# Optimization experiments

Hardware: AMD Instinct MI355X
Metric: run time of the kernel (lower is better)

The kernel has to match this reference:

```python
import jax, jax.numpy as jnp
import numpy as np

L, E, TOP_K = 3, 8, 2
B, N, D, DS = 256, 1024, 512, 128

def setup_inputs() -> dict:
    key = jax.random.key(0)
    ks = jax.random.split(key, 10)
    s = 0.05  # weight init scale
    return {
        "token": jax.random.normal(ks[0], (B, 1, D), jnp.float32),
        "node_emb": jax.random.normal(ks[1], (B, N, D), jnp.float32),
        "states": jnp.zeros((L, E, B, DS), jnp.float32),
        "Wg": jax.random.normal(ks[2], (L, D, E), jnp.float32) * s,
        "bg": jnp.zeros((L, E), jnp.float32),
        "A": jax.random.normal(ks[3], (L, E, DS), jnp.float32),
        "Bin": jax.random.normal(ks[4], (L, E, D, DS), jnp.float32) * s,
        "Cout": jax.random.normal(ks[5], (L, E, DS, D), jnp.float32) * s,
        "Dsk": jax.random.normal(ks[6], (L, E, D), jnp.float32) * s,
        "Wq": jax.random.normal(ks[7], (D, D), jnp.float32) * s,
        "bq": jnp.zeros((D,), jnp.float32),
    }

def reference(token, node_emb, states, Wg, bg, A, Bin, Cout, Dsk, Wq, bq):
    # token: (B,1,D) -> h: (B,D)
    h = token[:, 0, :]
    lb_loss = jnp.float32(0.0)
    new_states = []
    for l in range(L):
        # --- MoE router: top-k softmax gating ---
        probs = jax.nn.softmax(h @ Wg[l] + bg[l])              # (B,E)
        topv, topi = jax.lax.top_k(probs, TOP_K)               # (B,k)
        gates_k = topv / jnp.sum(topv, axis=-1, keepdims=True)  # renormalized
        oh = jax.nn.one_hot(topi, E, dtype=probs.dtype)        # (B,k,E)
        gate_full = jnp.einsum('bk,bke->be', gates_k, oh)      # (B,E)
        sel = jnp.sum(oh, axis=1) > 0                          # (B,E) bool
        # --- state-space experts (computed densely for all experts) ---
        s = states[l]                                          # (E,B,DS)
        decay = jax.nn.sigmoid(A[l])[:, None, :]               # (E,1,DS)
        s_new = decay * s + jnp.einsum('bd,eds->ebs', h, Bin[l])   # (E,B,DS)
        y = jnp.einsum('ebs,esd->ebd', s_new, Cout[l]) + h[None] * Dsk[l][:, None, :]
        out = jnp.einsum('be,ebd->bd', gate_full, y)           # weighted combine
        # only routed experts advance their state
        keep = sel.T[:, :, None]                               # (E,B,1)
        new_states.append(jnp.where(keep, s_new, s))
        # load-balance loss: E * sum_e mean(probs_e) * mean(frac routed to e)
        lb_loss = lb_loss + E * jnp.sum(jnp.mean(probs, axis=0) * jnp.mean(sel.astype(probs.dtype), axis=0))
        h = h + out                                            # residual
    # --- query projection + logits over nodes ---
    q = h @ Wq + bq                                            # (B,D)
    logits = jnp.einsum('bd,bnd->bn', q, node_emb) / jnp.sqrt(jnp.float32(D))
    return logits, jnp.stack(new_states), lb_loss
```

## Files before the change

kernel.cpp:

```cpp
#include <hip/hip_runtime.h>
#include <math.h>

#define LNUM 3
#define ENUM 8
#define TOPK 2
#define BSZ 256
#define NSZ 1024
#define DSZ 512
#define SSZ 128

typedef float f32x4 __attribute__((ext_vector_type(4)));

__global__ __launch_bounds__(1024, 2) void mega_kernel(
    const float* __restrict__ token,
    const float* __restrict__ node_emb,
    const float* __restrict__ states,
    const float* __restrict__ Wg,
    const float* __restrict__ bg,
    const float* __restrict__ A,
    const float* __restrict__ Bin,
    const float* __restrict__ Cout,
    const float* __restrict__ Dsk,
    const float* __restrict__ Wq,
    const float* __restrict__ bq,
    float* __restrict__ out_logits,
    float* __restrict__ out_states,
    float* __restrict__ acc)
{
    const int b = blockIdx.x;
    const int t = threadIdx.x;
    const int wave = t >> 6;
    const int lane = t & 63;

    __shared__ float h_s[DSZ];
    __shared__ float yacc_s[DSZ];
    __shared__ float snew_s[TOPK][SSZ];
    __shared__ float logit_s[ENUM];
    __shared__ f32x4 part4[1024];
    float* part = (float*)part4;

    if (t < DSZ) h_s[t] = token[b * DSZ + t];

    for (int l = 0; l < LNUM; ++l) {
        const float* Wg_l  = Wg  + (size_t)l * DSZ * ENUM;
        const float* bg_l  = bg  + (size_t)l * ENUM;
        const float* A_l   = A   + (size_t)l * ENUM * SSZ;
        const float* Bin_l = Bin + (size_t)l * ENUM * DSZ * SSZ;
        const float* Cou_l = Cout+ (size_t)l * ENUM * SSZ * DSZ;
        const float* Dsk_l = Dsk + (size_t)l * ENUM * DSZ;
        const float* st_l  = states     + (size_t)l * ENUM * BSZ * SSZ;
        float*       os_l  = out_states + (size_t)l * ENUM * BSZ * SSZ;

        __syncthreads();
        part4[t] = ((const f32x4*)Wg_l)[t];
        __syncthreads();

        if (wave < ENUM) {
            float p = 0.f;
            #pragma unroll
            for (int i = 0; i < 8; ++i) {
                const int d = lane + i * 64;
                p = fmaf(h_s[d], part[d * ENUM + wave], p);
            }
            for (int off = 32; off; off >>= 1) p += __shfl_down(p, off, 64);
            if (lane == 0) logit_s[wave] = p + bg_l[wave];
        }
        __syncthreads();

        float probs[ENUM];
        float mx = logit_s[0];
        for (int e = 1; e < ENUM; ++e) mx = fmaxf(mx, logit_s[e]);
        float ssum = 0.f;
        for (int e = 0; e < ENUM; ++e) { probs[e] = expf(logit_s[e] - mx); ssum += probs[e]; }
        const float sinv = 1.f / ssum;
        for (int e = 0; e < ENUM; ++e) probs[e] *= sinv;

        int i0 = 0;
        for (int e = 1; e < ENUM; ++e) if (probs[e] > probs[i0]) i0 = e;
        int i1 = -1;
        for (int e = 0; e < ENUM; ++e) {
            if (e == i0) continue;
            if (i1 < 0 || probs[e] > probs[i1]) i1 = e;
        }
        float g0 = probs[i0], g1 = probs[i1];
        const float ginv = 1.f / (g0 + g1);
        g0 *= ginv; g1 *= ginv;

        if (t < ENUM) {
            atomicAdd(&acc[(l * 2 + 0) * ENUM + t], probs[t]);
            atomicAdd(&acc[(l * 2 + 1) * ENUM + t], (t == i0 || t == i1) ? 1.0f : 0.0f);
        }

        #pragma unroll
        for (int k = 0; k < TOPK; ++k) {
            const int e = k ? i1 : i0;
            {
                const int c  = t >> 5;
                const int sq = t & 31;
                const float* Bp = Bin_l + (size_t)e * DSZ * SSZ + sq * 4;
                const int d0 = c * 16;
                f32x4 acc4 = {0.f, 0.f, 0.f, 0.f};
                #pragma unroll
                for (int d = 0; d < 16; ++d)
                    acc4 += *(const f32x4*)(Bp + (size_t)(d0 + d) * SSZ) * h_s[d0 + d];
                part4[c * 32 + sq] = acc4;
            }
            __syncthreads();
            if (t < SSZ) {
                float sum = 0.f;
                #pragma unroll
                for (int c = 0; c < 32; ++c) sum += part[c * 128 + t];
                const float a = A_l[e * SSZ + t];
                const float decay = 1.f / (1.f + expf(-a));
                snew_s[k][t] = decay * st_l[((size_t)e * BSZ + b) * SSZ + t] + sum;
            }
            __syncthreads();
        }

        {
            const int e = t >> 7, s = t & 127;
            float v;
            if (e == i0)      v = snew_s[0][s];
            else if (e == i1) v = snew_s[1][s];
            else              v = st_l[((size_t)e * BSZ + b) * SSZ + s];
            os_l[((size_t)e * BSZ + b) * SSZ + s] = v;
        }

        #pragma unroll
        for (int k = 0; k < TOPK; ++k) {
            const int e = k ? i1 : i0;
            const float g = k ? g1 : g0;
            {
                const int sc = t >> 7;
                const int dq = t & 127;
                const float* Cp = Cou_l + (size_t)e * SSZ * DSZ + dq * 4;
                const float* sp = snew_s[k];
                const int s0 = sc * 16;
                f32x4 acc4 = {0.f, 0.f, 0.f, 0.f};
                #pragma unroll
                for (int s = 0; s < 16; ++s)
                    acc4 += *(const f32x4*)(Cp + (size_t)(s0 + s) * DSZ) * sp[s0 + s];
                part4[sc * 128 + dq] = acc4;
            }
            __syncthreads();
            if (t < DSZ) {
                float yk = 0.f;
                #pragma unroll
                for (int sc = 0; sc < 8; ++sc) yk += part[sc * 512 + t];
                const float hd = h_s[t];
                yk = g * (yk + hd * Dsk_l[e * DSZ + t]);
                if (k == 0) yacc_s[t] = yk;
                else        h_s[t] = hd + yacc_s[t] + yk;
            }
            __syncthreads();
        }
    }

    {
        const int chunk = t >> 7;
        const int dquad = t & 127;
        const int dd0 = chunk * 64;
        f32x4 acc4 = {0.f, 0.f, 0.f, 0.f};
        #pragma unroll 8
        for (int i = 0; i < 64; ++i)
            acc4 += *(const f32x4*)(Wq + (size_t)(dd0 + i) * DSZ + dquad * 4) * h_s[dd0 + i];
        part4[chunk * 128 + dquad] = acc4;
    }
    __syncthreads();
    if (t < DSZ) {
        float qv = bq[t];
        #pragma unroll
        for (int c = 0; c < 8; ++c) qv += part[c * 512 + t];
        yacc_s[t] = qv;
    }
    __syncthreads();

    {
        const f32x4 q0 = ((const f32x4*)yacc_s)[lane];
        const f32x4 q1 = ((const f32x4*)yacc_s)[lane + 64];
        const float scale = 0.04419417382415922f;
        const int n0 = wave * 64;
        for (int i = 0; i < 64; i += 2) {
            const f32x4* r0 = (const f32x4*)(node_emb + ((size_t)b * NSZ + n0 + i) * DSZ);
            const f32x4* r1 = (const f32x4*)(node_emb + ((size_t)b * NSZ + n0 + i + 1) * DSZ);
            const f32x4 a0 = __builtin_nontemporal_load(r0 + lane);
            const f32x4 a1 = __builtin_nontemporal_load(r0 + lane + 64);
            const f32x4 c0 = __builtin_nontemporal_load(r1 + lane);
            const f32x4 c1 = __builtin_nontemporal_load(r1 + lane + 64);
            float d0 = a0.x*q0.x + a0.y*q0.y + a0.z*q0.z + a0.w*q0.w
                     + a1.x*q1.x + a1.y*q1.y + a1.z*q1.z + a1.w*q1.w;
            float d1 = c0.x*q0.x + c0.y*q0.y + c0.z*q0.z + c0.w*q0.w
                     + c1.x*q1.x + c1.y*q1.y + c1.z*q1.z + c1.w*q1.w;
            #pragma unroll
            for (int off = 32; off; off >>= 1) {
                d0 += __shfl_down(d0, off, 64);
                d1 += __shfl_down(d1, off, 64);
            }
            if (lane == 0) {
                out_logits[b * NSZ + n0 + i]     = d0 * scale;
                out_logits[b * NSZ + n0 + i + 1] = d1 * scale;
            }
        }
    }
}

__global__ void loss_kernel(const float* __restrict__ acc, float* __restrict__ out)
{
    if (threadIdx.x == 0) {
        float lb = 0.f;
        for (int l = 0; l < LNUM; ++l)
            for (int e = 0; e < ENUM; ++e) {
                const float mp = acc[(l * 2 + 0) * ENUM + e] * (1.0f / BSZ);
                const float ms = acc[(l * 2 + 1) * ENUM + e] * (1.0f / BSZ);
                lb += (float)ENUM * mp * ms;
            }
        out[0] = lb;
    }
}

extern "C" void kernel_launch(void* const* d_in, const int* in_sizes, int n_in,
                              void* d_out, int out_size, void* d_ws, size_t ws_size,
                              hipStream_t stream) {
    const float* token    = (const float*)d_in[0];
    const float* node_emb = (const float*)d_in[1];
    const float* states   = (const float*)d_in[2];
    const float* Wg       = (const float*)d_in[3];
    const float* bg       = (const float*)d_in[4];
    const float* A        = (const float*)d_in[5];
    const float* Bin      = (const float*)d_in[6];
    const float* Cout     = (const float*)d_in[7];
    const float* Dsk      = (const float*)d_in[8];
    const float* Wq       = (const float*)d_in[9];
    const float* bq       = (const float*)d_in[10];

    float* out_logits = (float*)d_out;
    float* out_states = out_logits + (size_t)BSZ * NSZ;
    float* out_loss   = out_states + (size_t)LNUM * ENUM * BSZ * SSZ;

    float* ws_acc = (float*)d_ws;

    (void)hipMemsetAsync(ws_acc, 0, sizeof(float) * LNUM * 16, stream);

    mega_kernel<<<BSZ, 1024, 0, stream>>>(
        token, node_emb, states, Wg, bg, A, Bin, Cout, Dsk, Wq, bq,
        out_logits, out_states, ws_acc);

    loss_kernel<<<1, 64, 0, stream>>>(ws_acc, out_loss);
}
```

Before: 160.1 us.

## Compute both top-k experts concurrently with shuffle reductions instead of LDS partials

Splits the 1024 threads into two halves so both selected experts' Bin and Cout matvecs run at the same time. Cross-thread partial sums are reduced with wave xor-shuffles rather than a shared-memory partial buffer, and the Wq projection gets the same treatment. This removes several __syncthreads barriers and the LDS round-trips per layer, and the Wg staging into shared memory is replaced by direct global reads. In exchange, each thread now runs a longer serial loop, the shuffle reductions cost extra instructions, and the reduced values are extracted with lane-dependent selects.

```diff
diff --git a/kernel.cpp b/kernel.cpp
--- a/kernel.cpp
+++ b/kernel.cpp
@@ -10,6 +10,15 @@
 #define SSZ 128
 
 typedef float f32x4 __attribute__((ext_vector_type(4)));
+
+__device__ __forceinline__ f32x4 shfl_xor4(f32x4 v, int mask) {
+    f32x4 r;
+    r.x = __shfl_xor(v.x, mask, 64);
+    r.y = __shfl_xor(v.y, mask, 64);
+    r.z = __shfl_xor(v.z, mask, 64);
+    r.w = __shfl_xor(v.w, mask, 64);
+    return r;
+}
 
 __global__ __launch_bounds__(1024, 2) void mega_kernel(
     const float* __restrict__ token,
@@ -33,11 +42,10 @@
     const int lane = t & 63;
 
     __shared__ float h_s[DSZ];
-    __shared__ float yacc_s[DSZ];
+    __shared__ float q_s[DSZ];
     __shared__ float snew_s[TOPK][SSZ];
+    __shared__ float ypart[TOPK][DSZ];
     __shared__ float logit_s[ENUM];
-    __shared__ f32x4 part4[1024];
-    float* part = (float*)part4;
 
     if (t < DSZ) h_s[t] = token[b * DSZ + t];
 
@@ -52,15 +60,12 @@
         float*       os_l  = out_states + (size_t)l * ENUM * BSZ * SSZ;
 
         __syncthreads();
-        part4[t] = ((const f32x4*)Wg_l)[t];
-        __syncthreads();
-
         if (wave < ENUM) {
             float p = 0.f;
             #pragma unroll
             for (int i = 0; i < 8; ++i) {
                 const int d = lane + i * 64;
-                p = fmaf(h_s[d], part[d * ENUM + wave], p);
+                p = fmaf(h_s[d], Wg_l[d * ENUM + wave], p);
             }
             for (int off = 32; off; off >>= 1) p += __shfl_down(p, off, 64);
             if (lane == 0) logit_s[wave] = p + bg_l[wave];
@@ -91,93 +96,97 @@
             atomicAdd(&acc[(l * 2 + 1) * ENUM + t], (t == i0 || t == i1) ? 1.0f : 0.0f);
         }
 
-        #pragma unroll
-        for (int k = 0; k < TOPK; ++k) {
-            const int e = k ? i1 : i0;
-            {
-                const int c  = t >> 5;
-                const int sq = t & 31;
-                const float* Bp = Bin_l + (size_t)e * DSZ * SSZ + sq * 4;
-                const int d0 = c * 16;
-                f32x4 acc4 = {0.f, 0.f, 0.f, 0.f};
-                #pragma unroll
-                for (int d = 0; d < 16; ++d)
-                    acc4 += *(const f32x4*)(Bp + (size_t)(d0 + d) * SSZ) * h_s[d0 + d];
-                part4[c * 32 + sq] = acc4;
-            }
-            __syncthreads();
-            if (t < SSZ) {
-                float sum = 0.f;
-                #pragma unroll
-                for (int c = 0; c < 32; ++c) sum += part[c * 128 + t];
-                const float a = A_l[e * SSZ + t];
+        {
+            const int k  = t >> 9;
+            const int r  = t & 511;
+            const int sq = r >> 4;
+            const int kc = r & 15;
+            const int e  = k ? i1 : i0;
+            const float* Bp = Bin_l + (size_t)e * DSZ * SSZ + (size_t)(kc * 32) * SSZ + sq * 4;
+            const float* hp = h_s + kc * 32;
+            f32x4 a0 = {0.f,0.f,0.f,0.f}, a1 = a0;
+            #pragma unroll 4
+            for (int d = 0; d < 32; d += 2) {
+                a0 += *(const f32x4*)(Bp + (size_t)d * SSZ) * hp[d];
+                a1 += *(const f32x4*)(Bp + (size_t)(d + 1) * SSZ) * hp[d + 1];
+            }
+            f32x4 s4 = a0 + a1;
+            s4 += shfl_xor4(s4, 1);
+            s4 += shfl_xor4(s4, 2);
+            s4 += shfl_xor4(s4, 4);
+            s4 += shfl_xor4(s4, 8);
+            if (kc < 4) {
+                const int s = sq * 4 + kc;
+                const float sum = (kc == 0) ? s4.x : (kc == 1) ? s4.y : (kc == 2) ? s4.z : s4.w;
+                const float a = A_l[e * SSZ + s];
                 const float decay = 1.f / (1.f + expf(-a));
-                snew_s[k][t] = decay * st_l[((size_t)e * BSZ + b) * SSZ + t] + sum;
-            }
-            __syncthreads();
-        }
-
+                const float sn = decay * st_l[((size_t)e * BSZ + b) * SSZ + s] + sum;
+                snew_s[k][s] = sn;
+                os_l[((size_t)e * BSZ + b) * SSZ + s] = sn;
+            }
+        }
         {
             const int e = t >> 7, s = t & 127;
-            float v;
-            if (e == i0)      v = snew_s[0][s];
-            else if (e == i1) v = snew_s[1][s];
-            else              v = st_l[((size_t)e * BSZ + b) * SSZ + s];
-            os_l[((size_t)e * BSZ + b) * SSZ + s] = v;
-        }
-
-        #pragma unroll
-        for (int k = 0; k < TOPK; ++k) {
-            const int e = k ? i1 : i0;
-            const float g = k ? g1 : g0;
-            {
-                const int sc = t >> 7;
-                const int dq = t & 127;
-                const float* Cp = Cou_l + (size_t)e * SSZ * DSZ + dq * 4;
-                const float* sp = snew_s[k];
-                const int s0 = sc * 16;
-                f32x4 acc4 = {0.f, 0.f, 0.f, 0.f};
-                #pragma unroll
-                for (int s = 0; s < 16; ++s)
-                    acc4 += *(const f32x4*)(Cp + (size_t)(s0 + s) * DSZ) * sp[s0 + s];
-                part4[sc * 128 + dq] = acc4;
-            }
-            __syncthreads();
-            if (t < DSZ) {
-                float yk = 0.f;
-                #pragma unroll
-                for (int sc = 0; sc < 8; ++sc) yk += part[sc * 512 + t];
-                const float hd = h_s[t];
-                yk = g * (yk + hd * Dsk_l[e * DSZ + t]);
-                if (k == 0) yacc_s[t] = yk;
-                else        h_s[t] = hd + yacc_s[t] + yk;
-            }
-            __syncthreads();
-        }
-    }
-
+            if (e != i0 && e != i1)
+                os_l[((size_t)e * BSZ + b) * SSZ + s] = st_l[((size_t)e * BSZ + b) * SSZ + s];
+        }
+        __syncthreads();
+
+        {
+            const int k  = t >> 9;
+            const int r  = t & 511;
+            const int dq = r >> 2;
+            const int sc = r & 3;
+            const int e  = k ? i1 : i0;
+            const float* Cp = Cou_l + (size_t)e * SSZ * DSZ + (size_t)(sc * 32) * DSZ + dq * 4;
+            const float* sp = snew_s[k] + sc * 32;
+            f32x4 a0 = {0.f,0.f,0.f,0.f}, a1 = a0;
+            #pragma unroll 4
+            for (int s = 0; s < 32; s += 2) {
+                a0 += *(const f32x4*)(Cp + (size_t)s * DSZ) * sp[s];
+                a1 += *(const f32x4*)(Cp + (size_t)(s + 1) * DSZ) * sp[s + 1];
+            }
+            f32x4 s4 = a0 + a1;
+            s4 += shfl_xor4(s4, 1);
+            s4 += shfl_xor4(s4, 2);
+            const float yv = (sc == 0) ? s4.x : (sc == 1) ? s4.y : (sc == 2) ? s4.z : s4.w;
+            ypart[k][dq * 4 + sc] = yv;
+        }
+        __syncthreads();
+
+        if (t < DSZ) {
+            const float hd = h_s[t];
+            const float y0 = ypart[0][t] + hd * Dsk_l[i0 * DSZ + t];
+            const float y1 = ypart[1][t] + hd * Dsk_l[i1 * DSZ + t];
+            h_s[t] = hd + g0 * y0 + g1 * y1;
+        }
+    }
+
+    __syncthreads();
     {
-        const int chunk = t >> 7;
-        const int dquad = t & 127;
-        const int dd0 = chunk * 64;
-        f32x4 acc4 = {0.f, 0.f, 0.f, 0.f};
-        #pragma unroll 8
-        for (int i = 0; i < 64; ++i)
-            acc4 += *(const f32x4*)(Wq + (size_t)(dd0 + i) * DSZ + dquad * 4) * h_s[dd0 + i];
-        part4[chunk * 128 + dquad] = acc4;
+        const int dq = t >> 3, kc = t & 7;
+        const float* Wp = Wq + (size_t)(kc * 64) * DSZ + dq * 4;
+        const float* hp = h_s + kc * 64;
+        f32x4 a0 = {0.f,0.f,0.f,0.f}, a1 = a0;
+        #pragma unroll 4
+        for (int i = 0; i < 64; i += 2) {
+            a0 += *(const f32x4*)(Wp + (size_t)i * DSZ) * hp[i];
+            a1 += *(const f32x4*)(Wp + (size_t)(i + 1) * DSZ) * hp[i + 1];
+        }
+        f32x4 s4 = a0 + a1;
+        s4 += shfl_xor4(s4, 1);
+        s4 += shfl_xor4(s4, 2);
+        s4 += shfl_xor4(s4, 4);
+        if (kc < 4) {
+            const int d = dq * 4 + kc;
+            q_s[d] = ((kc == 0) ? s4.x : (kc == 1) ? s4.y : (kc == 2) ? s4.z : s4.w) + bq[d];
+        }
     }
     __syncthreads();
-    if (t < DSZ) {
-        float qv = bq[t];
-        #pragma unroll
-        for (int c = 0; c < 8; ++c) qv += part[c * 512 + t];
-        yacc_s[t] = qv;
-    }
-    __syncthreads();
 
     {
-        const f32x4 q0 = ((const f32x4*)yacc_s)[lane];
-        const f32x4 q1 = ((const f32x4*)yacc_s)[lane + 64];
+        const f32x4 q0 = ((const f32x4*)q_s)[lane];
+        const f32x4 q1 = ((const f32x4*)q_s)[lane + 64];
         const float scale = 0.04419417382415922f;
         const int n0 = wave * 64;
         for (int i = 0; i < 64; i += 2) {
```

After: 232.9 us. 45.5% more time.

## Process both top-k experts concurrently across block halves to halve barrier phases

Applied to the files above, without the earlier changes.

Instead of looping over the two selected experts sequentially, the block is split into two halves of 512 threads, each computing the Bin and Cout matvecs for one expert at the same time, with longer per-thread reduction chunks and two accumulators. The state write-back is merged into the s_new computation, and the two expert outputs are combined in one final pass. This removes several __syncthreads phases per layer and increases memory-level parallelism for the weight reads, at the cost of slightly more work per thread.

```diff
diff --git a/kernel.cpp b/kernel.cpp
--- a/kernel.cpp
+++ b/kernel.cpp
@@ -31,15 +31,16 @@
     const int t = threadIdx.x;
     const int wave = t >> 6;
     const int lane = t & 63;
+    const int ehalf = t >> 9;
 
     __shared__ float h_s[DSZ];
-    __shared__ float yacc_s[DSZ];
+    __shared__ float q_s[DSZ];
     __shared__ float snew_s[TOPK][SSZ];
     __shared__ float logit_s[ENUM];
     __shared__ f32x4 part4[1024];
     float* part = (float*)part4;
 
-    if (t < DSZ) h_s[t] = token[b * DSZ + t];
+    if (t < 128) ((f32x4*)h_s)[t] = ((const f32x4*)(token + (size_t)b * DSZ))[t];
 
     for (int l = 0; l < LNUM; ++l) {
         const float* Wg_l  = Wg  + (size_t)l * DSZ * ENUM;
@@ -90,72 +91,74 @@
             atomicAdd(&acc[(l * 2 + 0) * ENUM + t], probs[t]);
             atomicAdd(&acc[(l * 2 + 1) * ENUM + t], (t == i0 || t == i1) ? 1.0f : 0.0f);
         }
-
-        #pragma unroll
-        for (int k = 0; k < TOPK; ++k) {
+        const int esel = ehalf ? i1 : i0;
+
+        {
+            const int rem = t & 511;
+            const int c   = rem >> 5;
+            const int sq  = rem & 31;
+            const float* Bp = Bin_l + (size_t)esel * DSZ * SSZ + sq * 4;
+            const int d0 = c * 32;
+            f32x4 a0 = {0.f,0.f,0.f,0.f}, a1 = a0;
+            #pragma unroll 8
+            for (int d = 0; d < 32; d += 2) {
+                a0 += *(const f32x4*)(Bp + (size_t)(d0 + d) * SSZ) * h_s[d0 + d];
+                a1 += *(const f32x4*)(Bp + (size_t)(d0 + d + 1) * SSZ) * h_s[d0 + d + 1];
+            }
+            part4[(ehalf * 16 + c) * 32 + sq] = a0 + a1;
+        }
+        __syncthreads();
+
+        if (t < TOPK * SSZ) {
+            const int k = t >> 7, s = t & 127;
             const int e = k ? i1 : i0;
-            {
-                const int c  = t >> 5;
-                const int sq = t & 31;
-                const float* Bp = Bin_l + (size_t)e * DSZ * SSZ + sq * 4;
-                const int d0 = c * 16;
-                f32x4 acc4 = {0.f, 0.f, 0.f, 0.f};
-                #pragma unroll
-                for (int d = 0; d < 16; ++d)
-                    acc4 += *(const f32x4*)(Bp + (size_t)(d0 + d) * SSZ) * h_s[d0 + d];
-                part4[c * 32 + sq] = acc4;
-            }
-            __syncthreads();
-            if (t < SSZ) {
-                float sum = 0.f;
-                #pragma unroll
-                for (int c = 0; c < 32; ++c) sum += part[c * 128 + t];
-                const float a = A_l[e * SSZ + t];
-                const float decay = 1.f / (1.f + expf(-a));
-                snew_s[k][t] = decay * st_l[((size_t)e * BSZ + b) * SSZ + t] + sum;
-            }
-            __syncthreads();
-        }
-
+            float sum = 0.f;
+            #pragma unroll
+            for (int c = 0; c < 16; ++c) sum += part[(k * 16 + c) * 128 + s];
+            const float a = A_l[e * SSZ + s];
+            const float decay = 1.f / (1.f + expf(-a));
+            const float sn = decay * st_l[((size_t)e * BSZ + b) * SSZ + s] + sum;
+            snew_s[k][s] = sn;
+            os_l[((size_t)e * BSZ + b) * SSZ + s] = sn;
+        }
         {
             const int e = t >> 7, s = t & 127;
-            float v;
-            if (e == i0)      v = snew_s[0][s];
-            else if (e == i1) v = snew_s[1][s];
-            else              v = st_l[((size_t)e * BSZ + b) * SSZ + s];
-            os_l[((size_t)e * BSZ + b) * SSZ + s] = v;
-        }
-
-        #pragma unroll
-        for (int k = 0; k < TOPK; ++k) {
-            const int e = k ? i1 : i0;
-            const float g = k ? g1 : g0;
-            {
-                const int sc = t >> 7;
-                const int dq = t & 127;
-                const float* Cp = Cou_l + (size_t)e * SSZ * DSZ + dq * 4;
-                const float* sp = snew_s[k];
-                const int s0 = sc * 16;
-                f32x4 acc4 = {0.f, 0.f, 0.f, 0.f};
-                #pragma unroll
-                for (int s = 0; s < 16; ++s)
-                    acc4 += *(const f32x4*)(Cp + (size_t)(s0 + s) * DSZ) * sp[s0 + s];
-                part4[sc * 128 + dq] = acc4;
-            }
-            __syncthreads();
-            if (t < DSZ) {
-                float yk = 0.f;
-                #pragma unroll
-                for (int sc = 0; sc < 8; ++sc) yk += part[sc * 512 + t];
-                const float hd = h_s[t];
-                yk = g * (yk + hd * Dsk_l[e * DSZ + t]);
-                if (k == 0) yacc_s[t] = yk;
-                else        h_s[t] = hd + yacc_s[t] + yk;
-            }
-            __syncthreads();
-        }
-    }
-
+            if (e != i0 && e != i1)
+                os_l[((size_t)e * BSZ + b) * SSZ + s] = st_l[((size_t)e * BSZ + b) * SSZ + s];
+        }
+        __syncthreads();
+
+        {
+            const int rem = t & 511;
+            const int sc  = rem >> 7;
+            const int dq  = rem & 127;
+            const float* Cp = Cou_l + (size_t)esel * SSZ * DSZ + dq * 4;
+            const float* sp = snew_s[ehalf];
+            const int s0 = sc * 32;
+            f32x4 a0 = {0.f,0.f,0.f,0.f}, a1 = a0;
+            #pragma unroll 8
+            for (int s = 0; s < 32; s += 2) {
+                a0 += *(const f32x4*)(Cp + (size_t)(s0 + s) * DSZ) * sp[s0 + s];
+                a1 += *(const f32x4*)(Cp + (size_t)(s0 + s + 1) * DSZ) * sp[s0 + s + 1];
+            }
+            part4[(ehalf * 4 + sc) * 128 + dq] = a0 + a1;
+        }
+        __syncthreads();
+
+        if (t < DSZ) {
+            const float hd = h_s[t];
+            float y0 = hd * Dsk_l[i0 * DSZ + t];
+            float y1 = hd * Dsk_l[i1 * DSZ + t];
+            #pragma unroll
+            for (int c = 0; c < 4; ++c) {
+                y0 += part[c * 512 + t];
+                y1 += part[(4 + c) * 512 + t];
+            }
+            h_s[t] = hd + g0 * y0 + g1 * y1;
+        }
+    }
+
+    __syncthreads();
     {
         const int chunk = t >> 7;
         const int dquad = t & 127;
@@ -171,13 +174,13 @@
         float qv = bq[t];
         #pragma unroll
         for (int c = 0; c < 8; ++c) qv += part[c * 512 + t];
-        yacc_s[t] = qv;
+        q_s[t] = qv;
     }
     __syncthreads();
 
     {
-        const f32x4 q0 = ((const f32x4*)yacc_s)[lane];
-        const f32x4 q1 = ((const f32x4*)yacc_s)[lane + 64];
+        const f32x4 q0 = ((const f32x4*)q_s)[lane];
+        const f32x4 q1 = ((const f32x4*)q_s)[lane + 64];
         const float scale = 0.04419417382415922f;
         const int n0 = wave * 64;
         for (int i = 0; i < 64; i += 2) {
```

Result: slower. 166.3 us (+3.9%).
